# Kernel tuning notes

Hardware: AMD Instinct MI355X
Metric: run time of the kernel (lower is better)

## Reference

```python
import jax, jax.numpy as jnp
import numpy as np

BETA = 2.0  # config.beta_start (beta_anneal=True, step 0)


def _generate_e8_roots() -> np.ndarray:
    roots = []
    # 112 integer roots: (+-1, +-1, 0^6) in all index pairs
    for i in range(8):
        for j in range(i + 1, 8):
            for si in (1.0, -1.0):
                for sj in (1.0, -1.0):
                    v = np.zeros(8, dtype=np.float32)
                    v[i] = si
                    v[j] = sj
                    roots.append(v)
    # 128 half-integer roots: (+-1/2)^8 with even number of minus signs
    for bits in range(256):
        signs = np.array([1.0 if ((bits >> k) & 1) == 0 else -1.0 for k in range(8)], dtype=np.float32)
        if int((signs < 0).sum()) % 2 == 0:
            roots.append(0.5 * signs)
    return np.stack(roots)  # [240, 8], each of norm sqrt(2)


def setup_inputs() -> dict:
    key = jax.random.key(0)
    ks = jax.random.split(key, 4)
    B, S, D_Q, H, D_K, N_SLOTS, D_V = 4, 65536, 14, 32, 8, 240, 256
    query = jax.random.normal(ks[0], (B, S, D_Q), dtype=jnp.float32)
    # orthogonal-ish init approximated with scaled gaussians (math path identical)
    W1 = jax.random.normal(ks[1], (H, D_Q), dtype=jnp.float32) * (1.0 / np.sqrt(D_Q))
    b1 = jnp.zeros((H,), dtype=jnp.float32)
    W2 = jax.random.normal(ks[2], (D_K, H), dtype=jnp.float32) * (1.0 / np.sqrt(H))
    b2 = jnp.zeros((D_K,), dtype=jnp.float32)
    values = jax.random.normal(ks[3], (N_SLOTS, D_V), dtype=jnp.float32) * 0.02
    roots = _generate_e8_roots()
    keys_n = jnp.asarray(roots / np.linalg.norm(roots, axis=-1, keepdims=True))
    return {"query": query, "W1": W1, "b1": b1, "W2": W2, "b2": b2,
            "values": values, "keys_n": keys_n}


def reference(query, W1, b1, W2, b2, values, keys_n):
    # flatten [B,S,D] -> [N,D] as in read()
    x = query.reshape(-1, query.shape[-1])
    # G2Projection: Linear(14,32) -> GELU (exact) -> Linear(32,8) -> L2 normalize
    h = jax.nn.gelu(x @ W1.T + b1, approximate=False)
    q8 = h @ W2.T + b2
    q8 = q8 / jnp.maximum(jnp.linalg.norm(q8, axis=-1, keepdims=True), 1e-12)
    # Hopfield attention over 240 normalized E8 root keys
    sim = q8 @ keys_n.T                      # [N, 240]
    attn = jax.nn.softmax(BETA * sim, axis=-1)
    content = attn @ values                  # [N, 256]
    return content, attn
```

## Files before the change

### kernel.cpp

```cpp
#include <hip/hip_runtime.h>
#include <math.h>

#define DQ 14
#define HD 32
#define DK 8
#define NK 240
#define DV 256
#define RB 64
#define NT 512
#define NFRAG 65536

typedef __attribute__((ext_vector_type(8))) short bf16x8;
typedef __attribute__((ext_vector_type(4))) float f32x4;

__device__ __forceinline__ unsigned bf16_rn(float x) {
    unsigned u = __float_as_uint(x);
    return (u + 0x7fffu + ((u >> 16) & 1u)) >> 16;
}

__global__ void prep_values(const float* __restrict__ values,
                            unsigned short* __restrict__ ws_hi,
                            unsigned short* __restrict__ ws_lo) {
    int idx = blockIdx.x * 256 + threadIdx.x;
    int e  = idx & 7;
    int l  = (idx >> 3) & 63;
    int ks = (idx >> 9) & 7;
    int nt = idx >> 12;
    int k = ks * 32 + ((l >> 4) << 3) + e;
    int n = nt * 16 + (l & 15);
    float v = (k < NK) ? values[k * DV + n] : 0.0f;
    unsigned hb = bf16_rn(v);
    float hf = __uint_as_float(hb << 16);
    unsigned lb = bf16_rn(v - hf);
    ws_hi[idx] = (unsigned short)hb;
    ws_lo[idx] = (unsigned short)lb;
}

__global__ __launch_bounds__(NT, 4)
void em_fused(const float* __restrict__ query,
              const float* __restrict__ W1, const float* __restrict__ b1,
              const float* __restrict__ W2, const float* __restrict__ b2,
              const float* __restrict__ keys,
              const unsigned short* __restrict__ ws_hi,
              const unsigned short* __restrict__ ws_lo,
              float* __restrict__ out_content, float* __restrict__ out_attn)
{
    __shared__ float s_x[RB][DQ];
    __shared__ float s_h[RB][HD + 1];
    __shared__ float s_q8[RB][DK + 1];
    __shared__ __align__(16) unsigned short s_Ah[RB * 256];
    __shared__ __align__(16) unsigned short s_Al[RB * 256];

    const int tid = threadIdx.x;
    const long row0 = (long)blockIdx.x * RB;

    for (int e = tid; e < RB * DQ; e += NT) {
        s_x[e / DQ][e % DQ] = query[row0 * DQ + e];
    }
    __syncthreads();

    #pragma unroll
    for (int it = 0; it < (RB * HD) / NT; ++it) {
        int task = it * NT + tid;
        int r = task >> 5, j = task & 31;
        float acc = b1[j];
        #pragma unroll
        for (int c = 0; c < DQ; ++c) acc += s_x[r][c] * W1[j * DQ + c];
        s_h[r][j] = 0.5f * acc * (1.0f + erff(acc * 0.70710678118654752f));
    }
    __syncthreads();

    {
        int r = tid >> 3, i = tid & 7;
        float acc = b2[i];
        #pragma unroll
        for (int c = 0; c < HD; ++c) acc += s_h[r][c] * W2[i * HD + c];
        s_q8[r][i] = acc;
    }
    __syncthreads();

    if (tid < RB) {
        float ss = 0.f;
        #pragma unroll
        for (int i = 0; i < DK; ++i) { float v = s_q8[tid][i]; ss += v * v; }
        float inv = 1.0f / fmaxf(sqrtf(ss), 1e-12f);
        #pragma unroll
        for (int i = 0; i < DK; ++i) s_q8[tid][i] *= inv;
    }
    __syncthreads();

    {
        const int wv = tid >> 6, lane = tid & 63;
        const int t0 = lane * 4;
        float kr[4][DK];
        #pragma unroll
        for (int s = 0; s < 4; ++s) {
            #pragma unroll
            for (int c = 0; c < DK; ++c)
                kr[s][c] = (t0 + s < NK) ? keys[(t0 + s) * DK + c] : 0.0f;
        }
        char* ahp = (char*)s_Ah;
        char* alp = (char*)s_Al;
        for (int rr = 0; rr < 8; ++rr) {
            const int r = wv * 8 + rr;
            float q[DK];
            #pragma unroll
            for (int c = 0; c < DK; ++c) q[c] = s_q8[r][c];
            float ex[4];
            float ssum = 0.f;
            #pragma unroll
            for (int s = 0; s < 4; ++s) {
                float sim = 0.f;
                #pragma unroll
                for (int c = 0; c < DK; ++c) sim += q[c] * kr[s][c];
                float v = (t0 + s < NK) ? __expf(2.0f * sim) : 0.0f;
                ex[s] = v;
                ssum += v;
            }
            #pragma unroll
            for (int m = 1; m < 64; m <<= 1) ssum += __shfl_xor(ssum, m, 64);
            const float inv = 1.0f / ssum;
            float a0 = ex[0] * inv, a1 = ex[1] * inv, a2 = ex[2] * inv, a3 = ex[3] * inv;
            if (t0 < NK) {
                *(float4*)&out_attn[(row0 + r) * NK + t0] =
                    make_float4(a0, a1, a2, a3);
            }
            unsigned h0 = bf16_rn(a0), h1 = bf16_rn(a1), h2 = bf16_rn(a2), h3 = bf16_rn(a3);
            float f0 = __uint_as_float(h0 << 16), f1 = __uint_as_float(h1 << 16);
            float f2 = __uint_as_float(h2 << 16), f3 = __uint_as_float(h3 << 16);
            unsigned l0 = bf16_rn(a0 - f0), l1 = bf16_rn(a1 - f1);
            unsigned l2 = bf16_rn(a2 - f2), l3 = bf16_rn(a3 - f3);
            unsigned off = ((unsigned)(r * 512 + lane * 8)) ^ (((unsigned)(r & 7)) << 4);
            *(ushort4*)(ahp + off) = make_ushort4((unsigned short)h0, (unsigned short)h1,
                                                  (unsigned short)h2, (unsigned short)h3);
            *(ushort4*)(alp + off) = make_ushort4((unsigned short)l0, (unsigned short)l1,
                                                  (unsigned short)l2, (unsigned short)l3);
        }
    }
    __syncthreads();

    {
        const int wv = tid >> 6, lane = tid & 63;
        const int l15 = lane & 15, l4 = lane >> 4;
        f32x4 acc[4][2];
        #pragma unroll
        for (int i = 0; i < 4; ++i)
            #pragma unroll
            for (int j = 0; j < 2; ++j)
                acc[i][j] = (f32x4){0.f, 0.f, 0.f, 0.f};

        const char* ahp = (const char*)s_Ah;
        const char* alp = (const char*)s_Al;
        const bf16x8* Vh = (const bf16x8*)ws_hi;
        const bf16x8* Vl = (const bf16x8*)ws_lo;

        #pragma unroll
        for (int ks = 0; ks < 8; ++ks) {
            bf16x8 vh[2], vl[2], ah[4], al[4];
            #pragma unroll
            for (int ntl = 0; ntl < 2; ++ntl) {
                int fi = (((wv * 2 + ntl) * 8 + ks) << 6) + lane;
                vh[ntl] = Vh[fi];
                vl[ntl] = Vl[fi];
            }
            #pragma unroll
            for (int mt = 0; mt < 4; ++mt) {
                int m = mt * 16 + l15;
                unsigned off = ((unsigned)(m * 512 + ks * 64 + l4 * 16)) ^
                               (((unsigned)(m & 7)) << 4);
                ah[mt] = *(const bf16x8*)(ahp + off);
                al[mt] = *(const bf16x8*)(alp + off);
            }
            #pragma unroll
            for (int ntl = 0; ntl < 2; ++ntl) {
                #pragma unroll
                for (int mt = 0; mt < 4; ++mt) {
                    acc[mt][ntl] = __builtin_amdgcn_mfma_f32_16x16x32_bf16(
                        vh[ntl], ah[mt], acc[mt][ntl], 0, 0, 0);
                    acc[mt][ntl] = __builtin_amdgcn_mfma_f32_16x16x32_bf16(
                        vl[ntl], ah[mt], acc[mt][ntl], 0, 0, 0);
                    acc[mt][ntl] = __builtin_amdgcn_mfma_f32_16x16x32_bf16(
                        vh[ntl], al[mt], acc[mt][ntl], 0, 0, 0);
                }
            }
        }

        #pragma unroll
        for (int mt = 0; mt < 4; ++mt) {
            const long row = row0 + mt * 16 + l15;
            #pragma unroll
            for (int ntl = 0; ntl < 2; ++ntl) {
                const int n = (wv * 2 + ntl) * 16 + l4 * 4;
                float4 o = make_float4(acc[mt][ntl][0], acc[mt][ntl][1],
                                       acc[mt][ntl][2], acc[mt][ntl][3]);
                *(float4*)&out_content[row * DV + n] = o;
            }
        }
    }
}

extern "C" void kernel_launch(void* const* d_in, const int* in_sizes, int n_in,
                              void* d_out, int out_size, void* d_ws, size_t ws_size,
                              hipStream_t stream) {
    const float* query  = (const float*)d_in[0];
    const float* W1     = (const float*)d_in[1];
    const float* b1     = (const float*)d_in[2];
    const float* W2     = (const float*)d_in[3];
    const float* b2     = (const float*)d_in[4];
    const float* values = (const float*)d_in[5];
    const float* keys   = (const float*)d_in[6];

    const int nrows = in_sizes[0] / DQ;
    float* out_content = (float*)d_out;
    float* out_attn    = out_content + (size_t)nrows * DV;

    unsigned short* wh = (unsigned short*)d_ws;
    unsigned short* wl = wh + NFRAG;

    prep_values<<<NFRAG / 256, 256, 0, stream>>>(values, wh, wl);
    em_fused<<<nrows / RB, NT, 0, stream>>>(query, W1, b1, W2, b2, keys,
                                            wh, wl, out_content, out_attn);
}
```

Baseline: 697.9 us.

## Split fused kernel into projection/softmax kernel and content MFMA kernel

```diff
diff --git a/kernel.cpp b/kernel.cpp
--- a/kernel.cpp
+++ b/kernel.cpp
@@ -7,7 +7,6 @@
 #define NK 240
 #define DV 256
 #define RB 64
-#define NT 512
 #define NFRAG 65536
 
 typedef __attribute__((ext_vector_type(8))) short bf16x8;
@@ -36,32 +35,28 @@
     ws_lo[idx] = (unsigned short)lb;
 }
 
-__global__ __launch_bounds__(NT, 4)
-void em_fused(const float* __restrict__ query,
-              const float* __restrict__ W1, const float* __restrict__ b1,
-              const float* __restrict__ W2, const float* __restrict__ b2,
-              const float* __restrict__ keys,
-              const unsigned short* __restrict__ ws_hi,
-              const unsigned short* __restrict__ ws_lo,
-              float* __restrict__ out_content, float* __restrict__ out_attn)
+__global__ __launch_bounds__(256, 4)
+void em_proj(const float* __restrict__ query,
+             const float* __restrict__ W1, const float* __restrict__ b1,
+             const float* __restrict__ W2, const float* __restrict__ b2,
+             const float* __restrict__ keys,
+             float* __restrict__ out_attn)
 {
     __shared__ float s_x[RB][DQ];
     __shared__ float s_h[RB][HD + 1];
     __shared__ float s_q8[RB][DK + 1];
-    __shared__ __align__(16) unsigned short s_Ah[RB * 256];
-    __shared__ __align__(16) unsigned short s_Al[RB * 256];
 
     const int tid = threadIdx.x;
     const long row0 = (long)blockIdx.x * RB;
 
-    for (int e = tid; e < RB * DQ; e += NT) {
+    for (int e = tid; e < RB * DQ; e += 256) {
         s_x[e / DQ][e % DQ] = query[row0 * DQ + e];
     }
     __syncthreads();
 
     #pragma unroll
-    for (int it = 0; it < (RB * HD) / NT; ++it) {
-        int task = it * NT + tid;
+    for (int it = 0; it < (RB * HD) / 256; ++it) {
+        int task = it * 256 + tid;
         int r = task >> 5, j = task & 31;
         float acc = b1[j];
         #pragma unroll
@@ -70,8 +65,10 @@
     }
     __syncthreads();
 
-    {
-        int r = tid >> 3, i = tid & 7;
+    #pragma unroll
+    for (int it = 0; it < (RB * DK) / 256; ++it) {
+        int task = it * 256 + tid;
+        int r = task >> 3, i = task & 7;
         float acc = b2[i];
         #pragma unroll
         for (int c = 0; c < HD; ++c) acc += s_h[r][c] * W2[i * HD + c];
@@ -99,10 +96,8 @@
             for (int c = 0; c < DK; ++c)
                 kr[s][c] = (t0 + s < NK) ? keys[(t0 + s) * DK + c] : 0.0f;
         }
-        char* ahp = (char*)s_Ah;
-        char* alp = (char*)s_Al;
-        for (int rr = 0; rr < 8; ++rr) {
-            const int r = wv * 8 + rr;
+        for (int rr = 0; rr < 16; ++rr) {
+            const int r = wv * 16 + rr;
             float q[DK];
             #pragma unroll
             for (int c = 0; c < DK; ++c) q[c] = s_q8[r][c];
@@ -120,16 +115,44 @@
             #pragma unroll
             for (int m = 1; m < 64; m <<= 1) ssum += __shfl_xor(ssum, m, 64);
             const float inv = 1.0f / ssum;
-            float a0 = ex[0] * inv, a1 = ex[1] * inv, a2 = ex[2] * inv, a3 = ex[3] * inv;
             if (t0 < NK) {
                 *(float4*)&out_attn[(row0 + r) * NK + t0] =
-                    make_float4(a0, a1, a2, a3);
-            }
-            unsigned h0 = bf16_rn(a0), h1 = bf16_rn(a1), h2 = bf16_rn(a2), h3 = bf16_rn(a3);
+                    make_float4(ex[0] * inv, ex[1] * inv, ex[2] * inv, ex[3] * inv);
+            }
+        }
+    }
+}
+
+__global__ __launch_bounds__(512, 4)
+void em_content(const float* __restrict__ attn_in,
+                const unsigned short* __restrict__ ws_hi,
+                const unsigned short* __restrict__ ws_lo,
+                float* __restrict__ out_content)
+{
+    __shared__ __align__(16) unsigned short s_Ah[RB * 256];
+    __shared__ __align__(16) unsigned short s_Al[RB * 256];
+
+    const int tid = threadIdx.x;
+    const int wv = tid >> 6, lane = tid & 63;
+    const long row0 = (long)blockIdx.x * RB;
+
+    {
+        char* ahp = (char*)s_Ah;
+        char* alp = (char*)s_Al;
+        const int t0 = lane * 4;
+        #pragma unroll
+        for (int rr = 0; rr < 8; ++rr) {
+            const int r = wv * 8 + rr;
+            float4 a = make_float4(0.f, 0.f, 0.f, 0.f);
+            if (t0 < NK) {
+                a = *(const float4*)&attn_in[(row0 + r) * NK + t0];
+            }
+            unsigned h0 = bf16_rn(a.x), h1 = bf16_rn(a.y),
+                     h2 = bf16_rn(a.z), h3 = bf16_rn(a.w);
             float f0 = __uint_as_float(h0 << 16), f1 = __uint_as_float(h1 << 16);
             float f2 = __uint_as_float(h2 << 16), f3 = __uint_as_float(h3 << 16);
-            unsigned l0 = bf16_rn(a0 - f0), l1 = bf16_rn(a1 - f1);
-            unsigned l2 = bf16_rn(a2 - f2), l3 = bf16_rn(a3 - f3);
+            unsigned l0 = bf16_rn(a.x - f0), l1 = bf16_rn(a.y - f1);
+            unsigned l2 = bf16_rn(a.z - f2), l3 = bf16_rn(a.w - f3);
             unsigned off = ((unsigned)(r * 512 + lane * 8)) ^ (((unsigned)(r & 7)) << 4);
             *(ushort4*)(ahp + off) = make_ushort4((unsigned short)h0, (unsigned short)h1,
                                                   (unsigned short)h2, (unsigned short)h3);
@@ -140,7 +163,6 @@
     __syncthreads();
 
     {
-        const int wv = tid >> 6, lane = tid & 63;
         const int l15 = lane & 15, l4 = lane >> 4;
         f32x4 acc[4][2];
         #pragma unroll
@@ -218,6 +240,6 @@
     unsigned short* wl = wh + NFRAG;
 
     prep_values<<<NFRAG / 256, 256, 0, stream>>>(values, wh, wl);
-    em_fused<<<nrows / RB, NT, 0, stream>>>(query, W1, b1, W2, b2, keys,
-                                            wh, wl, out_content, out_attn);
-}
+    em_proj<<<nrows / RB, 256, 0, stream>>>(query, W1, b1, W2, b2, keys, out_attn);
+    em_content<<<nrows / RB, 512, 0, stream>>>(out_attn, wh, wl, out_content);
+}
```

Result: slower. 734.0 us (+5.2%).
